# Performance work log

Measured on AMD Instinct MI355X. Metric: run time of the kernel, lower is better.

The kernel has to match this reference:

```python
import jax, jax.numpy as jnp
import numpy as np

B, S, H, DH, W, G, M = 2, 4096, 12, 64, 256, 64, 256
D = H * DH  # 768
VOCAB = 50282
NEG = -1e9


def setup_inputs() -> dict:
    key = jax.random.key(0)
    ks = jax.random.split(key, 16)
    f = lambda k, shp, s=0.02: jax.random.normal(k, shp, jnp.float32) * s
    return {
        'input_ids': jax.random.randint(ks[0], (B, S), 0, VOCAB, jnp.int32),
        'attn_mask': jnp.ones((B, S), jnp.float32),
        'html_idx': jnp.sort(jax.random.randint(ks[1], (B, M), 0, S, jnp.int32), axis=-1),
        'embed': f(ks[2], (VOCAB, D), 1.0),
        'Wq': f(ks[3], (D, D)), 'bq': jnp.zeros((D,), jnp.float32),
        'Wk': f(ks[4], (D, D)), 'bk': jnp.zeros((D,), jnp.float32),
        'Wv': f(ks[5], (D, D)), 'bv': jnp.zeros((D,), jnp.float32),
        'Wo': f(ks[6], (D, D)), 'bo': jnp.zeros((D,), jnp.float32),
        'gamma': jnp.ones((D,), jnp.float32), 'beta': jnp.zeros((D,), jnp.float32),
        'Wp': f(ks[7], (D, D)), 'bp': jnp.zeros((D,), jnp.float32),
        'Wa': f(ks[8], (D, 3)), 'ba': jnp.zeros((3,), jnp.float32),
        'Ws': f(ks[9], (D, 2)), 'bs': jnp.zeros((2,), jnp.float32),
    }


def _band_shift(t, n_chunks):
    # t: [..., n_chunks+2, W, ...chunked along axis -3/-2]; gather 3 neighbor chunks
    return jnp.concatenate([t[..., i:i + n_chunks, :, :] for i in range(3)], axis=-2)


def longformer_hpt(input_ids, attn_mask, html_idx, embed, Wq, bq, Wk, bk, Wv, bv,
                   Wo, bo, gamma, beta, Wp, bp, Wa, ba, Ws, bs):
    x = embed[input_ids]  # [B,S,D]
    heads = lambda t: t.reshape(B, S, H, DH).transpose(0, 2, 1, 3)  # [B,H,S,DH]
    q, k, v = heads(x @ Wq + bq), heads(x @ Wk + bk), heads(x @ Wv + bv)
    scale = 1.0 / np.sqrt(DH).astype(np.float32)
    C = S // W  # chunks

    # --- sliding-window (banded) attention, one-sided window W ---
    kp = jnp.pad(k, ((0, 0), (0, 0), (W, W), (0, 0))).reshape(B, H, C + 2, W, DH)
    vp = jnp.pad(v, ((0, 0), (0, 0), (W, W), (0, 0))).reshape(B, H, C + 2, W, DH)
    k3 = _band_shift(kp, C)  # [B,H,C,3W,DH]
    v3 = _band_shift(vp, C)
    qc = q.reshape(B, H, C, W, DH)
    sb = jnp.einsum('bhcqd,bhckd->bhcqk', qc, k3) * scale  # [B,H,C,W,3W]

    ii = jnp.arange(W)[:, None]
    jj = jnp.arange(3 * W)[None, :]
    band_ok = jnp.abs(jj - W - ii) <= W  # [W,3W]
    keypos = jnp.arange(C)[:, None] * W - W + jnp.arange(3 * W)[None, :]  # [C,3W]
    kvalid = (keypos >= 0) & (keypos < S) & (keypos >= G)  # global keys handled separately
    mp = jnp.pad(attn_mask, ((0, 0), (W, W))).reshape(B, C + 2, W)
    m3 = jnp.concatenate([mp[:, i:i + C] for i in range(3)], axis=2)  # [B,C,3W]
    mask = band_ok[None, :, :] & kvalid[:, None, :] & (m3[:, :, None, :] > 0)[..., :, :].reshape(B, C, 1, 3 * W).astype(bool) if False else (band_ok[None, None, :, :] & kvalid[None, :, None, :] & (m3[:, :, None, :] > 0))  # [B,C,W,3W]
    sb = jnp.where(mask[:, None], sb, NEG).reshape(B, H, S, 3 * W)

    # --- all tokens also attend to the G global tokens ---
    kg, vg = k[:, :, :G], v[:, :, :G]
    sg = jnp.einsum('bhsd,bhgd->bhsg', q, kg) * scale
    sg = jnp.where(attn_mask[:, None, None, :G] > 0, sg, NEG)

    p = jax.nn.softmax(jnp.concatenate([sg, sb], -1), -1)  # [B,H,S,G+3W]
    pg, pb = p[..., :G], p[..., G:].reshape(B, H, C, W, 3 * W)
    out = (jnp.einsum('bhcqk,bhckd->bhcqd', pb, v3).reshape(B, H, S, DH)
           + jnp.einsum('bhsg,bhgd->bhsd', pg, vg))

    # --- global queries attend to everything ---
    sgl = jnp.einsum('bhgd,bhsd->bhgs', q[:, :, :G], k) * scale
    sgl = jnp.where(attn_mask[:, None, None, :] > 0, sgl, NEG)
    outg = jnp.einsum('bhgs,bhsd->bhgd', jax.nn.softmax(sgl, -1), v)
    out = jnp.concatenate([outg, out[:, :, G:]], axis=2)

    ctx = out.transpose(0, 2, 1, 3).reshape(B, S, D)
    h = x + ctx @ Wo + bo
    mu = h.mean(-1, keepdims=True)
    var = ((h - mu) ** 2).mean(-1, keepdims=True)
    hn = (h - mu) / jnp.sqrt(var + 1e-5) * gamma + beta  # last_hidden [B,S,D]

    # probes (ans_probe: Linear(768,3)+Sigmoid, span_probe: Linear(768,2)+Sigmoid)
    ans = jax.nn.sigmoid(hn @ Wa + ba)
    span = jax.nn.sigmoid(hn @ Ws + bs)

    # ReIndexer gather of HTML-element hidden states + ConditionCalculator
    hr = jnp.take_along_axis(hn, html_idx[:, :, None].astype(jnp.int32), axis=1)  # [B,M,D]
    t = jax.nn.relu(hr @ Wp + bp)
    cond = jax.nn.sigmoid(jnp.einsum('bqh,bch->bcq', hr, t))  # [B,M,M]
    return hn, ans, span, cond


def reference(input_ids, attn_mask, html_idx, embed, Wq, bq, Wk, bk, Wv, bv,
              Wo, bo, gamma, beta, Wp, bp, Wa, ba, Ws, bs):
    return longformer_hpt(input_ids, attn_mask, html_idx, embed, Wq, bq, Wk, bk,
                          Wv, bv, Wo, bo, gamma, beta, Wp, bp, Wa, ba, Ws, bs)
```

## Files before the change

### kernel.cpp

```cpp
#include <hip/hip_runtime.h>

typedef unsigned short u16;
typedef unsigned int   u32;
typedef __attribute__((ext_vector_type(8))) short s8v;
typedef __attribute__((ext_vector_type(8))) unsigned short us8;
typedef __attribute__((ext_vector_type(4))) float f4v;

constexpr int BC  = 2;
constexpr int SL  = 4096;
constexpr int NH  = 12;
constexpr int HD  = 64;
constexpr int DM  = 768;
constexpr int WIN = 256;
constexpr int GLB = 64;
constexpr int QN  = 2304;
constexpr int KCH = 32;
constexpr float FOLD = 0.125f * 1.44269504088896f;
constexpr float NEGS = -1.0e9f;

__device__ __forceinline__ float b2f(u16 b){ return __uint_as_float(((u32)b) << 16); }
__device__ __forceinline__ u16 f2b(float f){
  u32 u = __float_as_uint(f);
  return (u16)((u + 0x7fffu + ((u >> 16) & 1u)) >> 16);
}
__device__ __forceinline__ float wredsum(float v){
  #pragma unroll
  for (int o = 32; o > 0; o >>= 1) v += __shfl_xor(v, o, 64);
  return v;
}
__device__ __forceinline__ float sigf(float x){ return 1.f / (1.f + __expf(-x)); }

__global__ void pack_embed(const float* __restrict__ Wq, const float* __restrict__ Wk,
                           const float* __restrict__ Wv, const float* __restrict__ Wo,
                           const float* __restrict__ Wp,
                           const float* __restrict__ bq, const float* __restrict__ bk,
                           const float* __restrict__ bv,
                           u16* __restrict__ wt_qkv, u16* __restrict__ wt_o,
                           u16* __restrict__ wt_p, float* __restrict__ b_qkv,
                           const int* __restrict__ ids, const float* __restrict__ emb,
                           u16* __restrict__ xb)
{
  __shared__ float tile[64][65];
  const int bid = blockIdx.x;
  const int t = threadIdx.x;
  if (bid < 720){
    const int mi = bid / 144, rest = bid % 144;
    const int kt = rest / 12, ntc = rest % 12;
    const float* src = (mi==0)?Wq:(mi==1)?Wk:(mi==2)?Wv:(mi==3)?Wo:Wp;
    u16* dst = (mi<3) ? (wt_qkv + (size_t)mi*768*768) : ((mi==3) ? wt_o : wt_p);
    const int k0 = kt*64, n0 = ntc*64;
    #pragma unroll
    for (int i=0;i<4;i++){
      const int r = (t>>4) + i*16;
      float4 v = ((const float4*)(src + (long)(k0+r)*768 + n0))[t&15];
      tile[r][(t&15)*4+0] = v.x; tile[r][(t&15)*4+1] = v.y;
      tile[r][(t&15)*4+2] = v.z; tile[r][(t&15)*4+3] = v.w;
    }
    __syncthreads();
    const int n = t & 63, kc = (t>>6)*16;
    u32* d32 = (u32*)(dst + (long)(n0+n)*768 + k0 + kc);
    #pragma unroll
    for (int i=0;i<8;i++){
      d32[i] = (u32)f2b(tile[kc+2*i][n]) | ((u32)f2b(tile[kc+2*i+1][n]) << 16);
    }
    if (bid < 9){
      const int i = bid*256 + t;
      if (i < 2304) b_qkv[i] = (i < 768) ? bq[i] : (i < 1536) ? bk[i-768] : bv[i-1536];
    }
  } else {
    int e4 = (bid-720)*256 + t;
    int row = e4 / 192, d4 = e4 - row*192;
    int id = ids[row];
    float4 v = ((const float4*)(emb + (long)id*768))[d4];
    u32 p0 = (u32)f2b(v.x) | ((u32)f2b(v.y) << 16);
    u32 p1 = (u32)f2b(v.z) | ((u32)f2b(v.w) << 16);
    ((u32*)(xb + (long)row*768))[d4*2]   = p0;
    ((u32*)(xb + (long)row*768))[d4*2+1] = p1;
  }
}

__global__ void gather_hr(const int* __restrict__ hidx, const float* __restrict__ hn,
                          u16* __restrict__ hrb){
  int e = blockIdx.x*256 + threadIdx.x;
  if (e >= 512*768) return;
  int r = e / 768, d = e - r*768;
  int b = r >> 8;
  int idx = hidx[r];
  hrb[e] = f2b(hn[((long)(b*SL + idx))*768 + d]);
}

template<int MODE, bool SWZ>
__global__ __launch_bounds__(256, 2)
void gemm_bt(const u16* __restrict__ A, const u16* __restrict__ Bt,
             const float* __restrict__ bias, const u16* __restrict__ resB,
             float* __restrict__ outF, u16* __restrict__ outB,
             int M, int N, int K, long sA, long sB, long sO)
{
  const int bz = blockIdx.z;
  A  += (long)bz * sA;
  Bt += (long)bz * sB;
  int vid = blockIdx.x + gridDim.x*blockIdx.y;
  if constexpr (SWZ){
    const int chunk = (gridDim.x*gridDim.y) >> 3;
    vid = (vid & 7)*chunk + (vid >> 3);
  }
  const int n0 = (vid % gridDim.x) * 128;
  const int m0 = (vid / gridDim.x) * 128;
  __shared__ u16 lsA[128*64];
  __shared__ u16 lsB[128*64];
  const int t = threadIdx.x;
  const int w = t >> 6, lane = t & 63;
  const int wr = w >> 1, wc = w & 1;
  const int fr = lane & 15, fq = lane >> 4;

  f4v acc[4][4];
  #pragma unroll
  for (int i=0;i<4;i++)
    #pragma unroll
    for (int j=0;j<4;j++) acc[i][j] = (f4v)0.f;

  for (int k0 = 0; k0 < K; k0 += 64){
    #pragma unroll
    for (int i=0;i<4;i++){
      int e = (w*4+i)*512 + lane*8;
      int row = e >> 6, col = e & 63;
      __builtin_amdgcn_global_load_lds(
        (const __attribute__((address_space(1))) void*)(A + (long)(m0+row)*K + (k0+col)),
        (__attribute__((address_space(3))) void*)(&lsA[(w*4+i)*512]), 16, 0, 0);
      __builtin_amdgcn_global_load_lds(
        (const __attribute__((address_space(1))) void*)(Bt + (long)(n0+row)*K + (k0+col)),
        (__attribute__((address_space(3))) void*)(&lsB[(w*4+i)*512]), 16, 0, 0);
    }
    __syncthreads();
    #pragma unroll
    for (int kk = 0; kk < 2; kk++){
      s8v af[4], bfv[4];
      #pragma unroll
      for (int mi=0;mi<4;mi++)
        af[mi] = *(const s8v*)&lsA[(wr*64 + mi*16 + fr)*64 + kk*32 + fq*8];
      #pragma unroll
      for (int ni=0;ni<4;ni++)
        bfv[ni] = *(const s8v*)&lsB[(wc*64 + ni*16 + fr)*64 + kk*32 + fq*8];
      #pragma unroll
      for (int mi=0;mi<4;mi++)
        #pragma unroll
        for (int ni=0;ni<4;ni++)
          acc[mi][ni] = __builtin_amdgcn_mfma_f32_16x16x32_bf16(af[mi], bfv[ni], acc[mi][ni], 0, 0, 0);
    }
    __syncthreads();
  }
  #pragma unroll
  for (int mi=0;mi<4;mi++){
    #pragma unroll
    for (int ni=0;ni<4;ni++){
      #pragma unroll
      for (int r=0;r<4;r++){
        int row = m0 + wr*64 + mi*16 + fq*4 + r;
        int col = n0 + wc*64 + ni*16 + fr;
        float v = acc[mi][ni][r];
        if constexpr (MODE == 0){
          v += bias[col];
          outB[(long)row*N + col] = f2b(v);
        } else if constexpr (MODE == 1){
          v += bias[col] + b2f(resB[(long)row*N + col]);
          outF[(long)row*N + col] = v;
        } else if constexpr (MODE == 2){
          v = fmaxf(v + bias[col], 0.f);
          outB[(long)row*N + col] = f2b(v);
        } else {
          (outF + bz*sO)[(long)row*N + col] = sigf(v);
        }
      }
    }
  }
}

__global__ __launch_bounds__(512, 2)
void attn_band_mfma(const u16* __restrict__ qkv, const float* __restrict__ mask, u16* __restrict__ ctx)
{
  const int bx = blockIdx.x;
  const int q0 = (((bx & 7) << 2) | (bx >> 3)) * 128;
  const int h = blockIdx.y, b = blockIdx.z;
  const int t = threadIdx.x;
  const int w = t >> 6, lane = t & 63;
  const int fq = lane >> 4, fr = lane & 15;
  const int qw = ((w >> 2) << 6) | ((w & 3) << 4);

  __shared__ u16 lsK[2][64*64];
  __shared__ u16 lsVT[2][64*72];
  __shared__ u16 lsP[8][16*72];
  __shared__ float lsM[2][64];

  const long bq = (long)b*SL*QN;
  const u16* qrow = qkv + (bq + (long)(q0 + qw + fr)*QN) + h*HD;
  s8v aq[2];
  aq[0] = *(const s8v*)(qrow + fq*8);
  aq[1] = *(const s8v*)(qrow + 32 + fq*8);

  const u16* kq = qkv + bq + DM + h*HD;
  const u16* vq = qkv + bq + 2*DM + h*HD;
  const float* mrow = mask + b*SL;

  const int kb0 = (q0 < 320) ? 64 : (q0 - 256);
  const int khi = (q0 + 384 < SL) ? (q0 + 384) : SL;
  const int NTT = 1 + ((khi - kb0) >> 6);

  f4v out[4];
  #pragma unroll
  for (int n=0;n<4;n++) out[n] = (f4v)0.f;
  float m[4]  = {-3.0e38f,-3.0e38f,-3.0e38f,-3.0e38f};
  float l[4]  = {0.f,0.f,0.f,0.f};

  us8 vv;
  auto stage_issue = [&](int i, int buf){
    const int k0 = (i == 0) ? 0 : kb0 + (i-1)*64;
    if (t < 64) lsM[buf][t] = mrow[k0 + t];
    const int r = w*8 + (lane>>3);
    const int d = ((lane&7) ^ (lane>>3))*8;
    __builtin_amdgcn_global_load_lds(
      (const __attribute__((address_space(1))) void*)(kq + (long)(k0+r)*QN + d),
      (__attribute__((address_space(3))) void*)(&lsK[buf][w*512]), 16, 0, 0);
    vv = *(const us8*)(vq + (long)(k0+lane)*QN + w*8);
  };

  stage_issue(0, 0);
  int cur = 0;
  for (int i = 0; i < NTT; i++){
    const int k0 = (i == 0) ? 0 : kb0 + (i-1)*64;
    const int d0 = w*8;
    #pragma unroll
    for (int jj=0;jj<8;jj++) lsVT[cur][(d0+jj)*72 + lane] = (u16)vv[jj];
    __syncthreads();
    if (i+1 < NTT) stage_issue(i+1, cur^1);

    f4v s[4];
    #pragma unroll
    for (int n=0;n<4;n++) s[n] = (f4v)0.f;
    __builtin_amdgcn_s_setprio(1);
    #pragma unroll
    for (int kk=0;kk<2;kk++){
      #pragma unroll
      for (int n=0;n<4;n++){
        s8v bf = *(const s8v*)&lsK[cur][(16*n+fr)*64 + (((kk*4+fq) ^ (fr&7))<<3)];
        s[n] = __builtin_amdgcn_mfma_f32_16x16x32_bf16(aq[kk], bf, s[n], 0,0,0);
      }
    }
    __builtin_amdgcn_s_setprio(0);
    const bool isg = (i == 0);
    #pragma unroll
    for (int n=0;n<4;n++){
      const int kcol = 16*n + fr;
      const float mk = lsM[cur][kcol];
      #pragma unroll
      for (int r=0;r<4;r++){
        const int dd = k0 + kcol - (q0 + qw + fq*4 + r);
        const bool valid = (mk > 0.f) && (isg || (dd >= -WIN && dd <= WIN));
        s[n][r] = valid ? s[n][r]*FOLD : NEGS;
      }
    }
    float rm[4];
    #pragma unroll
    for (int r=0;r<4;r++){
      float v = fmaxf(fmaxf(s[0][r], s[1][r]), fmaxf(s[2][r], s[3][r]));
      v = fmaxf(v, __shfl_xor(v, 1, 64));
      v = fmaxf(v, __shfl_xor(v, 2, 64));
      v = fmaxf(v, __shfl_xor(v, 4, 64));
      v = fmaxf(v, __shfl_xor(v, 8, 64));
      rm[r] = v;
    }
    bool need = false;
    #pragma unroll
    for (int r=0;r<4;r++) need |= (rm[r] > m[r] + 8.f);
    if (__any(need)){
      #pragma unroll
      for (int r=0;r<4;r++){
        const float mn = fmaxf(m[r], rm[r]);
        const float sf = exp2f(m[r] - mn);
        m[r] = mn;
        l[r] *= sf;
        #pragma unroll
        for (int n=0;n<4;n++) out[n][r] *= sf;
      }
    }
    u16* lsPw = lsP[w];
    float rs[4] = {0.f,0.f,0.f,0.f};
    #pragma unroll
    for (int n=0;n<4;n++){
      #pragma unroll
      for (int r=0;r<4;r++){
        float p = exp2f(s[n][r] - m[r]);
        rs[r] += p;
        lsPw[(fq*4+r)*72 + 16*n + fr] = f2b(p);
      }
    }
    #pragma unroll
    for (int r=0;r<4;r++){
      float rv = rs[r];
      rv += __shfl_xor(rv, 1, 64);
      rv += __shfl_xor(rv, 2, 64);
      rv += __shfl_xor(rv, 4, 64);
      rv += __shfl_xor(rv, 8, 64);
      l[r] += rv;
    }
    s8v ap[2];
    ap[0] = *(const s8v*)&lsPw[fr*72 + fq*8];
    ap[1] = *(const s8v*)&lsPw[fr*72 + 32 + fq*8];
    __builtin_amdgcn_s_setprio(1);
    #pragma unroll
    for (int kk=0;kk<2;kk++){
      #pragma unroll
      for (int n=0;n<4;n++){
        s8v bv = *(const s8v*)&lsVT[cur][(16*n+fr)*72 + kk*32 + fq*8];
        out[n] = __builtin_amdgcn_mfma_f32_16x16x32_bf16(ap[kk], bv, out[n], 0,0,0);
      }
    }
    __builtin_amdgcn_s_setprio(0);
    cur ^= 1;
  }
  #pragma unroll
  for (int r=0;r<4;r++) l[r] = 1.f/l[r];
  u16* cb = ctx + (((long)(b*SL) + q0 + qw + fq*4))*DM + h*HD + fr;
  #pragma unroll
  for (int n=0;n<4;n++)
    #pragma unroll
    for (int r=0;r<4;r++)
      cb[(long)r*DM + 16*n] = f2b(out[n][r]*l[r]);
}

__global__ __launch_bounds__(256, 3)
void attn_global_part(const u16* __restrict__ qkv, const float* __restrict__ mask,
                      float* __restrict__ pout, float* __restrict__ pml)
{
  const int ck = blockIdx.x;
  const int h = blockIdx.y, b = blockIdx.z;
  const int bh = b*NH + h;
  const int t = threadIdx.x;
  const int w = t >> 6, lane = t & 63;
  const int fq = lane >> 4, fr = lane & 15;

  __shared__ u16 lsK[2][64*64];
  __shared__ u16 lsVT[2][64*72];
  __shared__ u16 lsP[4][16*72];
  __shared__ float lsM[2][64];

  const long bq = (long)b*SL*QN;
  const u16* qrow = qkv + (bq + (long)(w*16 + fr)*QN) + h*HD;
  s8v aq[2];
  aq[0] = *(const s8v*)(qrow + fq*8);
  aq[1] = *(const s8v*)(qrow + 32 + fq*8);

  const u16* kq = qkv + bq + DM + h*HD;
  const u16* vq = qkv + bq + 2*DM + h*HD;
  const float* mrow = mask + b*SL;

  f4v out[4];
  #pragma unroll
  for (int n=0;n<4;n++) out[n] = (f4v)0.f;
  float m[4]  = {-3.0e38f,-3.0e38f,-3.0e38f,-3.0e38f};
  float l[4]  = {0.f,0.f,0.f,0.f};

  us8 vv0, vv1;
  auto stage_issue = [&](int i, int buf){
    const int k0 = ck*128 + i*64;
    if (t < 64) lsM[buf][t] = mrow[k0 + t];
    #pragma unroll
    for (int j=0;j<2;j++){
      const int r = (w*2+j)*8 + (lane>>3);
      const int d = ((lane&7) ^ (lane>>3))*8;
      __builtin_amdgcn_global_load_lds(
        (const __attribute__((address_space(1))) void*)(kq + (long)(k0+r)*QN + d),
        (__attribute__((address_space(3))) void*)(&lsK[buf][(w*2+j)*512]), 16, 0, 0);
    }
    vv0 = *(const us8*)(vq + (long)(k0+lane)*QN + w*8);
    vv1 = *(const us8*)(vq + (long)(k0+lane)*QN + w*8 + 32);
  };

  stage_issue(0, 0);
  int cur = 0;
  for (int i = 0; i < 2; i++){
    const int d0 = w*8;
    #pragma unroll
    for (int jj=0;jj<8;jj++) lsVT[cur][(d0+jj)*72 + lane] = (u16)vv0[jj];
    #pragma unroll
    for (int jj=0;jj<8;jj++) lsVT[cur][(d0+32+jj)*72 + lane] = (u16)vv1[jj];
    __syncthreads();
    if (i+1 < 2) stage_issue(i+1, cur^1);

    f4v s[4];
    #pragma unroll
    for (int n=0;n<4;n++) s[n] = (f4v)0.f;
    __builtin_amdgcn_s_setprio(1);
    #pragma unroll
    for (int kk=0;kk<2;kk++){
      #pragma unroll
      for (int n=0;n<4;n++){
        s8v bf = *(const s8v*)&lsK[cur][(16*n+fr)*64 + (((kk*4+fq) ^ (fr&7))<<3)];
        s[n] = __builtin_amdgcn_mfma_f32_16x16x32_bf16(aq[kk], bf, s[n], 0,0,0);
      }
    }
    __builtin_amdgcn_s_setprio(0);
    #pragma unroll
    for (int n=0;n<4;n++){
      const float mk = lsM[cur][16*n + fr];
      #pragma unroll
      for (int r=0;r<4;r++)
        s[n][r] = (mk > 0.f) ? s[n][r]*FOLD : NEGS;
    }
    float sf[4];
    #pragma unroll
    for (int r=0;r<4;r++){
      float rm = fmaxf(fmaxf(s[0][r], s[1][r]), fmaxf(s[2][r], s[3][r]));
      rm = fmaxf(rm, __shfl_xor(rm, 1, 64));
      rm = fmaxf(rm, __shfl_xor(rm, 2, 64));
      rm = fmaxf(rm, __shfl_xor(rm, 4, 64));
      rm = fmaxf(rm, __shfl_xor(rm, 8, 64));
      const float mn = fmaxf(m[r], rm);
      sf[r] = exp2f(m[r] - mn);
      m[r] = mn;
    }
    u16* lsPw = lsP[w];
    float rs[4] = {0.f,0.f,0.f,0.f};
    #pragma unroll
    for (int n=0;n<4;n++){
      #pragma unroll
      for (int r=0;r<4;r++){
        float p = exp2f(s[n][r] - m[r]);
        rs[r] += p;
        lsPw[(fq*4+r)*72 + 16*n + fr] = f2b(p);
        out[n][r] *= sf[r];
      }
    }
    #pragma unroll
    for (int r=0;r<4;r++){
      float rv = rs[r];
      rv += __shfl_xor(rv, 1, 64);
      rv += __shfl_xor(rv, 2, 64);
      rv += __shfl_xor(rv, 4, 64);
      rv += __shfl_xor(rv, 8, 64);
      l[r] = l[r]*sf[r] + rv;
    }
    s8v ap[2];
    ap[0] = *(const s8v*)&lsPw[fr*72 + fq*8];
    ap[1] = *(const s8v*)&lsPw[fr*72 + 32 + fq*8];
    __builtin_amdgcn_s_setprio(1);
    #pragma unroll
    for (int kk=0;kk<2;kk++){
      #pragma unroll
      for (int n=0;n<4;n++){
        s8v bv = *(const s8v*)&lsVT[cur][(16*n+fr)*72 + kk*32 + fq*8];
        out[n] = __builtin_amdgcn_mfma_f32_16x16x32_bf16(ap[kk], bv, out[n], 0,0,0);
      }
    }
    __builtin_amdgcn_s_setprio(0);
    cur ^= 1;
  }
  float* pob = pout + ((long)(ck*BC*NH + bh))*64*64;
  #pragma unroll
  for (int n=0;n<4;n++)
    #pragma unroll
    for (int r=0;r<4;r++)
      pob[(w*16 + fq*4 + r)*64 + 16*n + fr] = out[n][r];
  if (fr == 0){
    float* pmb = pml + ((long)(ck*BC*NH + bh))*128;
    #pragma unroll
    for (int r=0;r<4;r++){
      pmb[(w*16 + fq*4 + r)*2 + 0] = m[r];
      pmb[(w*16 + fq*4 + r)*2 + 1] = l[r];
    }
  }
}

__global__ __launch_bounds__(256, 2)
void attn_global_combine(const float* __restrict__ pout, const float* __restrict__ pml,
                         u16* __restrict__ ctx)
{
  const int bh = blockIdx.x;
  const int b = bh / NH, h = bh % NH;
  const int t = threadIdx.x;
  __shared__ float wgt[KCH][64];
  __shared__ float rl[64];
  if (t < 64){
    float mc[KCH], lc[KCH];
    #pragma unroll
    for (int c = 0; c < KCH; c++){
      const float* pmb = pml + ((long)(c*BC*NH + bh))*128 + t*2;
      mc[c] = pmb[0]; lc[c] = pmb[1];
    }
    float M = mc[0];
    #pragma unroll
    for (int c = 1; c < KCH; c++) M = fmaxf(M, mc[c]);
    float L = 0.f;
    #pragma unroll
    for (int c = 0; c < KCH; c++){
      const float wv = exp2f(mc[c] - M);
      wgt[c][t] = wv;
      L += lc[c]*wv;
    }
    rl[t] = 1.f/L;
  }
  __syncthreads();
  const int row = t >> 2, dseg = t & 3;
  float acc[16];
  #pragma unroll
  for (int i=0;i<16;i++) acc[i] = 0.f;
  for (int c = 0; c < KCH; c++){
    const float wv = wgt[c][row];
    const float4* pb = (const float4*)(pout + ((long)(c*BC*NH + bh)*64 + row)*64 + dseg*16);
    #pragma unroll
    for (int i = 0; i < 4; i++){
      float4 v = pb[i];
      acc[i*4+0] += v.x*wv; acc[i*4+1] += v.y*wv;
      acc[i*4+2] += v.z*wv; acc[i*4+3] += v.w*wv;
    }
  }
  u16* cr = ctx + ((long)(b*SL + row))*DM + h*HD + dseg*16;
  const float r = rl[row];
  #pragma unroll
  for (int i = 0; i < 16; i += 2){
    u32 pk = (u32)f2b(acc[i]*r) | ((u32)f2b(acc[i+1]*r) << 16);
    *(u32*)(cr + i) = pk;
  }
}

__global__ __launch_bounds__(256, 2)
void ln_heads(const float* __restrict__ hbuf, const float* __restrict__ gamma, const float* __restrict__ beta,
              const float* __restrict__ Wa, const float* __restrict__ ba,
              const float* __restrict__ Wsp, const float* __restrict__ bsp,
              float* __restrict__ hn, float* __restrict__ ans, float* __restrict__ span)
{
  const int r = blockIdx.x;
  const int t = threadIdx.x, lane = t & 63, w = t >> 6;
  __shared__ float red[8];
  __shared__ float dred[4][5];
  const float* hrow = hbuf + (long)r*DM;
  float v0 = hrow[t], v1 = hrow[t+256], v2 = hrow[t+512];
  float sum = wredsum(v0 + v1 + v2);
  float sq  = wredsum(v0*v0 + v1*v1 + v2*v2);
  if (lane == 0){ red[w] = sum; red[4+w] = sq; }
  __syncthreads();
  const float mu  = (red[0]+red[1]+red[2]+red[3]) * (1.f/768.f);
  const float msq = (red[4]+red[5]+red[6]+red[7]) * (1.f/768.f);
  const float rstd = rsqrtf(msq - mu*mu + 1e-5f);
  float pa0=0,pa1=0,pa2=0,ps0=0,ps1=0;
  const long base = (long)r*DM;
  #pragma unroll
  for (int jj = 0; jj < 3; jj++){
    const int i = t + jj*256;
    const float hv = (jj==0) ? v0 : (jj==1) ? v1 : v2;
    const float y = (hv - mu)*rstd*gamma[i] + beta[i];
    hn[base + i] = y;
    pa0 += y*Wa[i*3+0]; pa1 += y*Wa[i*3+1]; pa2 += y*Wa[i*3+2];
    ps0 += y*Wsp[i*2+0]; ps1 += y*Wsp[i*2+1];
  }
  pa0 = wredsum(pa0); pa1 = wredsum(pa1); pa2 = wredsum(pa2);
  ps0 = wredsum(ps0); ps1 = wredsum(ps1);
  if (lane == 0){ dred[w][0]=pa0; dred[w][1]=pa1; dred[w][2]=pa2; dred[w][3]=ps0; dred[w][4]=ps1; }
  __syncthreads();
  if (t == 0){
    float A0 = dred[0][0]+dred[1][0]+dred[2][0]+dred[3][0];
    float A1 = dred[0][1]+dred[1][1]+dred[2][1]+dred[3][1];
    float A2 = dred[0][2]+dred[1][2]+dred[2][2]+dred[3][2];
    float S0 = dred[0][3]+dred[1][3]+dred[2][3]+dred[3][3];
    float S1 = dred[0][4]+dred[1][4]+dred[2][4]+dred[3][4];
    ans[(long)r*3+0]  = sigf(A0 + ba[0]);
    ans[(long)r*3+1]  = sigf(A1 + ba[1]);
    ans[(long)r*3+2]  = sigf(A2 + ba[2]);
    span[(long)r*2+0] = sigf(S0 + bsp[0]);
    span[(long)r*2+1] = sigf(S1 + bsp[1]);
  }
}

extern "C" void kernel_launch(void* const* d_in, const int* in_sizes, int n_in,
                              void* d_out, int out_size, void* d_ws, size_t ws_size,
                              hipStream_t stream)
{
  const int*   input_ids = (const int*)  d_in[0];
  const float* attn_mask = (const float*)d_in[1];
  const int*   html_idx  = (const int*)  d_in[2];
  const float* embed     = (const float*)d_in[3];
  const float* Wq = (const float*)d_in[4];  const float* bq = (const float*)d_in[5];
  const float* Wk = (const float*)d_in[6];  const float* bk = (const float*)d_in[7];
  const float* Wv = (const float*)d_in[8];  const float* bv = (const float*)d_in[9];
  const float* Wo = (const float*)d_in[10]; const float* bo = (const float*)d_in[11];
  const float* gamma = (const float*)d_in[12]; const float* beta = (const float*)d_in[13];
  const float* Wp = (const float*)d_in[14]; const float* bp = (const float*)d_in[15];
  const float* Wa = (const float*)d_in[16]; const float* ba = (const float*)d_in[17];
  const float* Wsp = (const float*)d_in[18]; const float* bsp = (const float*)d_in[19];

  char* ws = (char*)d_ws;
  size_t off = 0;
  auto take = [&](size_t bytes)->char*{
    char* p = ws + off; off += (bytes + 255) & ~(size_t)255; return p;
  };
  u16*   x_b    = (u16*)  take((size_t)8192*768*2);
  u16*   wt_qkv = (u16*)  take((size_t)2304*768*2);
  u16*   wt_o   = (u16*)  take((size_t)768*768*2);
  u16*   wt_p   = (u16*)  take((size_t)768*768*2);
  float* b_qkv  = (float*)take(2304*4);
  u16*   qkv_b  = (u16*)  take((size_t)8192*2304*2);
  u16*   ctx_b  = (u16*)  take((size_t)8192*768*2);
  float* h_f    = (float*)take((size_t)8192*768*4);
  u16*   hr_b   = (u16*)  take((size_t)512*768*2);
  u16*   t_b    = (u16*)  take((size_t)512*768*2);
  float* pout   = (float*)take((size_t)KCH*BC*NH*64*64*4);
  float* pml    = (float*)take((size_t)KCH*BC*NH*128*4);

  float* out_hn   = (float*)d_out;
  float* out_ans  = out_hn  + (size_t)8192*768;
  float* out_span = out_ans + (size_t)8192*3;
  float* out_cond = out_span + (size_t)8192*2;

  pack_embed<<<6864, 256, 0, stream>>>(Wq, Wk, Wv, Wo, Wp, bq, bk, bv,
                                       wt_qkv, wt_o, wt_p, b_qkv,
                                       input_ids, embed, x_b);

  gemm_bt<0,true><<<dim3(18,64,1), 256, 0, stream>>>(x_b, wt_qkv, b_qkv, nullptr,
                                                nullptr, qkv_b, 8192, 2304, 768, 0,0,0);
  attn_band_mfma<<<dim3(32,12,2), 512, 0, stream>>>(qkv_b, attn_mask, ctx_b);
  attn_global_part<<<dim3(KCH,12,2), 256, 0, stream>>>(qkv_b, attn_mask, pout, pml);
  attn_global_combine<<<BC*NH, 256, 0, stream>>>(pout, pml, ctx_b);
  gemm_bt<1,true><<<dim3(6,64,1), 256, 0, stream>>>(ctx_b, wt_o, bo, x_b,
                                               h_f, nullptr, 8192, 768, 768, 0,0,0);
  ln_heads<<<8192, 256, 0, stream>>>(h_f, gamma, beta, Wa, ba, Wsp, bsp,
                                     out_hn, out_ans, out_span);
  gather_hr<<<1536, 256, 0, stream>>>(html_idx, out_hn, hr_b);
  gemm_bt<2,false><<<dim3(6,4,1), 256, 0, stream>>>(hr_b, wt_p, bp, nullptr,
                                              nullptr, t_b, 512, 768, 768, 0,0,0);
  gemm_bt<3,false><<<dim3(2,2,2), 256, 0, stream>>>(t_b, hr_b, nullptr, nullptr,
                                              out_cond, nullptr, 256, 256, 768,
                                              (long)256*768, (long)256*768, (long)256*256);
}
```

Measured before the change: 235.1 us.

## Fuse band and global attention into one launch; store pre-LN residual as bf16

```diff
diff --git a/kernel.cpp b/kernel.cpp
--- a/kernel.cpp
+++ b/kernel.cpp
@@ -163,7 +163,7 @@
           outB[(long)row*N + col] = f2b(v);
         } else if constexpr (MODE == 1){
           v += bias[col] + b2f(resB[(long)row*N + col]);
-          outF[(long)row*N + col] = v;
+          outB[(long)row*N + col] = f2b(v);
         } else if constexpr (MODE == 2){
           v = fmaxf(v + bias[col], 0.f);
           outB[(long)row*N + col] = f2b(v);
@@ -175,35 +175,26 @@
   }
 }
 
-__global__ __launch_bounds__(512, 2)
-void attn_band_mfma(const u16* __restrict__ qkv, const float* __restrict__ mask, u16* __restrict__ ctx)
+__global__ __launch_bounds__(256, 3)
+void attn_fused(const u16* __restrict__ qkv, const float* __restrict__ mask,
+                u16* __restrict__ ctx, float* __restrict__ pout, float* __restrict__ pml)
 {
   const int bx = blockIdx.x;
-  const int q0 = (((bx & 7) << 2) | (bx >> 3)) * 128;
+  const int vid = (bx & 7)*12 + (bx >> 3);
   const int h = blockIdx.y, b = blockIdx.z;
   const int t = threadIdx.x;
   const int w = t >> 6, lane = t & 63;
   const int fq = lane >> 4, fr = lane & 15;
-  const int qw = ((w >> 2) << 6) | ((w & 3) << 4);
 
   __shared__ u16 lsK[2][64*64];
   __shared__ u16 lsVT[2][64*72];
-  __shared__ u16 lsP[8][16*72];
+  __shared__ u16 lsP[4][16*72];
   __shared__ float lsM[2][64];
 
   const long bq = (long)b*SL*QN;
-  const u16* qrow = qkv + (bq + (long)(q0 + qw + fr)*QN) + h*HD;
-  s8v aq[2];
-  aq[0] = *(const s8v*)(qrow + fq*8);
-  aq[1] = *(const s8v*)(qrow + 32 + fq*8);
-
   const u16* kq = qkv + bq + DM + h*HD;
   const u16* vq = qkv + bq + 2*DM + h*HD;
   const float* mrow = mask + b*SL;
-
-  const int kb0 = (q0 < 320) ? 64 : (q0 - 256);
-  const int khi = (q0 + 384 < SL) ? (q0 + 384) : SL;
-  const int NTT = 1 + ((khi - kb0) >> 6);
 
   f4v out[4];
   #pragma unroll
@@ -211,261 +202,256 @@
   float m[4]  = {-3.0e38f,-3.0e38f,-3.0e38f,-3.0e38f};
   float l[4]  = {0.f,0.f,0.f,0.f};
 
-  us8 vv;
-  auto stage_issue = [&](int i, int buf){
-    const int k0 = (i == 0) ? 0 : kb0 + (i-1)*64;
-    if (t < 64) lsM[buf][t] = mrow[k0 + t];
-    const int r = w*8 + (lane>>3);
-    const int d = ((lane&7) ^ (lane>>3))*8;
-    __builtin_amdgcn_global_load_lds(
-      (const __attribute__((address_space(1))) void*)(kq + (long)(k0+r)*QN + d),
-      (__attribute__((address_space(3))) void*)(&lsK[buf][w*512]), 16, 0, 0);
-    vv = *(const us8*)(vq + (long)(k0+lane)*QN + w*8);
-  };
-
-  stage_issue(0, 0);
-  int cur = 0;
-  for (int i = 0; i < NTT; i++){
-    const int k0 = (i == 0) ? 0 : kb0 + (i-1)*64;
-    const int d0 = w*8;
-    #pragma unroll
-    for (int jj=0;jj<8;jj++) lsVT[cur][(d0+jj)*72 + lane] = (u16)vv[jj];
-    __syncthreads();
-    if (i+1 < NTT) stage_issue(i+1, cur^1);
-
-    f4v s[4];
-    #pragma unroll
-    for (int n=0;n<4;n++) s[n] = (f4v)0.f;
-    __builtin_amdgcn_s_setprio(1);
-    #pragma unroll
-    for (int kk=0;kk<2;kk++){
+  us8 vv0, vv1;
+
+  if (vid < 64){
+    const int q0 = vid * 64;
+    const u16* qrow = qkv + (bq + (long)(q0 + w*16 + fr)*QN) + h*HD;
+    s8v aq[2];
+    aq[0] = *(const s8v*)(qrow + fq*8);
+    aq[1] = *(const s8v*)(qrow + 32 + fq*8);
+
+    const int ti_lo = (q0 < 320) ? ((320 - q0) >> 6) : 0;
+    const int ti_hi_raw = (4352 - q0) >> 6;
+    const int ti_hi = ti_hi_raw < 9 ? ti_hi_raw : 9;
+    const int NTT = 1 + (ti_hi - ti_lo);
+    const int kb0 = q0 - 256 + ti_lo*64;
+
+    auto stage_issue = [&](int i, int buf){
+      const int k0 = (i == 0) ? 0 : kb0 + (i-1)*64;
+      if (t < 64) lsM[buf][t] = mrow[k0 + t];
+      #pragma unroll
+      for (int j=0;j<2;j++){
+        const int r = (w*2+j)*8 + (lane>>3);
+        const int d = ((lane&7) ^ (lane>>3))*8;
+        __builtin_amdgcn_global_load_lds(
+          (const __attribute__((address_space(1))) void*)(kq + (long)(k0+r)*QN + d),
+          (__attribute__((address_space(3))) void*)(&lsK[buf][(w*2+j)*512]), 16, 0, 0);
+      }
+      vv0 = *(const us8*)(vq + (long)(k0+lane)*QN + w*8);
+      vv1 = *(const us8*)(vq + (long)(k0+lane)*QN + w*8 + 32);
+    };
+
+    stage_issue(0, 0);
+    int cur = 0;
+    for (int i = 0; i < NTT; i++){
+      const int k0 = (i == 0) ? 0 : kb0 + (i-1)*64;
+      const int d0 = w*8;
+      #pragma unroll
+      for (int jj=0;jj<8;jj++) lsVT[cur][(d0+jj)*72 + lane] = (u16)vv0[jj];
+      #pragma unroll
+      for (int jj=0;jj<8;jj++) lsVT[cur][(d0+32+jj)*72 + lane] = (u16)vv1[jj];
+      __syncthreads();
+      if (i+1 < NTT) stage_issue(i+1, cur^1);
+
+      f4v s[4];
+      #pragma unroll
+      for (int n=0;n<4;n++) s[n] = (f4v)0.f;
+      __builtin_amdgcn_s_setprio(1);
+      #pragma unroll
+      for (int kk=0;kk<2;kk++){
+        #pragma unroll
+        for (int n=0;n<4;n++){
+          s8v bf = *(const s8v*)&lsK[cur][(16*n+fr)*64 + (((kk*4+fq) ^ (fr&7))<<3)];
+          s[n] = __builtin_amdgcn_mfma_f32_16x16x32_bf16(aq[kk], bf, s[n], 0,0,0);
+        }
+      }
+      __builtin_amdgcn_s_setprio(0);
+      const bool isg = (i == 0);
       #pragma unroll
       for (int n=0;n<4;n++){
-        s8v bf = *(const s8v*)&lsK[cur][(16*n+fr)*64 + (((kk*4+fq) ^ (fr&7))<<3)];
-        s[n] = __builtin_amdgcn_mfma_f32_16x16x32_bf16(aq[kk], bf, s[n], 0,0,0);
-      }
-    }
-    __builtin_amdgcn_s_setprio(0);
-    const bool isg = (i == 0);
-    #pragma unroll
-    for (int n=0;n<4;n++){
-      const int kcol = 16*n + fr;
-      const float mk = lsM[cur][kcol];
+        const int kcol = 16*n + fr;
+        const float mk = lsM[cur][kcol];
+        #pragma unroll
+        for (int r=0;r<4;r++){
+          const int dd = k0 + kcol - (q0 + w*16 + fq*4 + r);
+          const bool valid = (mk > 0.f) && (isg || (dd >= -WIN && dd <= WIN));
+          s[n][r] = valid ? s[n][r]*FOLD : NEGS;
+        }
+      }
+      float rm[4];
       #pragma unroll
       for (int r=0;r<4;r++){
-        const int dd = k0 + kcol - (q0 + qw + fq*4 + r);
-        const bool valid = (mk > 0.f) && (isg || (dd >= -WIN && dd <= WIN));
-        s[n][r] = valid ? s[n][r]*FOLD : NEGS;
-      }
-    }
-    float rm[4];
-    #pragma unroll
-    for (int r=0;r<4;r++){
-      float v = fmaxf(fmaxf(s[0][r], s[1][r]), fmaxf(s[2][r], s[3][r]));
-      v = fmaxf(v, __shfl_xor(v, 1, 64));
-      v = fmaxf(v, __shfl_xor(v, 2, 64));
-      v = fmaxf(v, __shfl_xor(v, 4, 64));
-      v = fmaxf(v, __shfl_xor(v, 8, 64));
-      rm[r] = v;
-    }
-    bool need = false;
-    #pragma unroll
-    for (int r=0;r<4;r++) need |= (rm[r] > m[r] + 8.f);
-    if (__any(need)){
+        float v = fmaxf(fmaxf(s[0][r], s[1][r]), fmaxf(s[2][r], s[3][r]));
+        v = fmaxf(v, __shfl_xor(v, 1, 64));
+        v = fmaxf(v, __shfl_xor(v, 2, 64));
+        v = fmaxf(v, __shfl_xor(v, 4, 64));
+        v = fmaxf(v, __shfl_xor(v, 8, 64));
+        rm[r] = v;
+      }
+      bool need = false;
+      #pragma unroll
+      for (int r=0;r<4;r++) need |= (rm[r] > m[r] + 8.f);
+      if (__any(need)){
+        #pragma unroll
+        for (int r=0;r<4;r++){
+          const float mn = fmaxf(m[r], rm[r]);
+          const float sf = exp2f(m[r] - mn);
+          m[r] = mn;
+          l[r] *= sf;
+          #pragma unroll
+          for (int n=0;n<4;n++) out[n][r] *= sf;
+        }
+      }
+      u16* lsPw = lsP[w];
+      float rs[4] = {0.f,0.f,0.f,0.f};
+      #pragma unroll
+      for (int n=0;n<4;n++){
+        #pragma unroll
+        for (int r=0;r<4;r++){
+          float p = exp2f(s[n][r] - m[r]);
+          rs[r] += p;
+          lsPw[(fq*4+r)*72 + 16*n + fr] = f2b(p);
+        }
+      }
       #pragma unroll
       for (int r=0;r<4;r++){
-        const float mn = fmaxf(m[r], rm[r]);
-        const float sf = exp2f(m[r] - mn);
+        float rv = rs[r];
+        rv += __shfl_xor(rv, 1, 64);
+        rv += __shfl_xor(rv, 2, 64);
+        rv += __shfl_xor(rv, 4, 64);
+        rv += __shfl_xor(rv, 8, 64);
+        l[r] += rv;
+      }
+      s8v ap[2];
+      ap[0] = *(const s8v*)&lsPw[fr*72 + fq*8];
+      ap[1] = *(const s8v*)&lsPw[fr*72 + 32 + fq*8];
+      __builtin_amdgcn_s_setprio(1);
+      #pragma unroll
+      for (int kk=0;kk<2;kk++){
+        #pragma unroll
+        for (int n=0;n<4;n++){
+          s8v bv = *(const s8v*)&lsVT[cur][(16*n+fr)*72 + kk*32 + fq*8];
+          out[n] = __builtin_amdgcn_mfma_f32_16x16x32_bf16(ap[kk], bv, out[n], 0,0,0);
+        }
+      }
+      __builtin_amdgcn_s_setprio(0);
+      cur ^= 1;
+    }
+    #pragma unroll
+    for (int r=0;r<4;r++) l[r] = 1.f/l[r];
+    u16* cb = ctx + (((long)(b*SL) + q0 + w*16 + fq*4))*DM + h*HD + fr;
+    #pragma unroll
+    for (int n=0;n<4;n++)
+      #pragma unroll
+      for (int r=0;r<4;r++)
+        cb[(long)r*DM + 16*n] = f2b(out[n][r]*l[r]);
+
+  } else {
+    const int ck = vid - 64;
+    const int bh = b*NH + h;
+    const u16* qrow = qkv + (bq + (long)(w*16 + fr)*QN) + h*HD;
+    s8v aq[2];
+    aq[0] = *(const s8v*)(qrow + fq*8);
+    aq[1] = *(const s8v*)(qrow + 32 + fq*8);
+
+    auto stage_issue = [&](int i, int buf){
+      const int k0 = ck*128 + i*64;
+      if (t < 64) lsM[buf][t] = mrow[k0 + t];
+      #pragma unroll
+      for (int j=0;j<2;j++){
+        const int r = (w*2+j)*8 + (lane>>3);
+        const int d = ((lane&7) ^ (lane>>3))*8;
+        __builtin_amdgcn_global_load_lds(
+          (const __attribute__((address_space(1))) void*)(kq + (long)(k0+r)*QN + d),
+          (__attribute__((address_space(3))) void*)(&lsK[buf][(w*2+j)*512]), 16, 0, 0);
+      }
+      vv0 = *(const us8*)(vq + (long)(k0+lane)*QN + w*8);
+      vv1 = *(const us8*)(vq + (long)(k0+lane)*QN + w*8 + 32);
+    };
+
+    stage_issue(0, 0);
+    int cur = 0;
+    for (int i = 0; i < 2; i++){
+      const int d0 = w*8;
+      #pragma unroll
+      for (int jj=0;jj<8;jj++) lsVT[cur][(d0+jj)*72 + lane] = (u16)vv0[jj];
+      #pragma unroll
+      for (int jj=0;jj<8;jj++) lsVT[cur][(d0+32+jj)*72 + lane] = (u16)vv1[jj];
+      __syncthreads();
+      if (i+1 < 2) stage_issue(i+1, cur^1);
+
+      f4v s[4];
+      #pragma unroll
+      for (int n=0;n<4;n++) s[n] = (f4v)0.f;
+      __builtin_amdgcn_s_setprio(1);
+      #pragma unroll
+      for (int kk=0;kk<2;kk++){
+        #pragma unroll
+        for (int n=0;n<4;n++){
+          s8v bf = *(const s8v*)&lsK[cur][(16*n+fr)*64 + (((kk*4+fq) ^ (fr&7))<<3)];
+          s[n] = __builtin_amdgcn_mfma_f32_16x16x32_bf16(aq[kk], bf, s[n], 0,0,0);
+        }
+      }
+      __builtin_amdgcn_s_setprio(0);
+      #pragma unroll
+      for (int n=0;n<4;n++){
+        const float mk = lsM[cur][16*n + fr];
+        #pragma unroll
+        for (int r=0;r<4;r++)
+          s[n][r] = (mk > 0.f) ? s[n][r]*FOLD : NEGS;
+      }
+      float sf[4];
+      #pragma unroll
+      for (int r=0;r<4;r++){
+        float rm = fmaxf(fmaxf(s[0][r], s[1][r]), fmaxf(s[2][r], s[3][r]));
+        rm = fmaxf(rm, __shfl_xor(rm, 1, 64));
+        rm = fmaxf(rm, __shfl_xor(rm, 2, 64));
+        rm = fmaxf(rm, __shfl_xor(rm, 4, 64));
+        rm = fmaxf(rm, __shfl_xor(rm, 8, 64));
+        const float mn = fmaxf(m[r], rm);
+        sf[r] = exp2f(m[r] - mn);
         m[r] = mn;
-        l[r] *= sf;
-        #pragma unroll
-        for (int n=0;n<4;n++) out[n][r] *= sf;
-      }
-    }
-    u16* lsPw = lsP[w];
-    float rs[4] = {0.f,0.f,0.f,0.f};
-    #pragma unroll
-    for (int n=0;n<4;n++){
+      }
+      u16* lsPw = lsP[w];
+      float rs[4] = {0.f,0.f,0.f,0.f};
+      #pragma unroll
+      for (int n=0;n<4;n++){
+        #pragma unroll
+        for (int r=0;r<4;r++){
+          float p = exp2f(s[n][r] - m[r]);
+          rs[r] += p;
+          lsPw[(fq*4+r)*72 + 16*n + fr] = f2b(p);
+          out[n][r] *= sf[r];
+        }
+      }
       #pragma unroll
       for (int r=0;r<4;r++){
-        float p = exp2f(s[n][r] - m[r]);
-        rs[r] += p;
-        lsPw[(fq*4+r)*72 + 16*n + fr] = f2b(p);
-      }
-    }
-    #pragma unroll
-    for (int r=0;r<4;r++){
-      float rv = rs[r];
-      rv += __shfl_xor(rv, 1, 64);
-      rv += __shfl_xor(rv, 2, 64);
-      rv += __shfl_xor(rv, 4, 64);
-      rv += __shfl_xor(rv, 8, 64);
-      l[r] += rv;
-    }
-    s8v ap[2];
-    ap[0] = *(const s8v*)&lsPw[fr*72 + fq*8];
-    ap[1] = *(const s8v*)&lsPw[fr*72 + 32 + fq*8];
-    __builtin_amdgcn_s_setprio(1);
-    #pragma unroll
-    for (int kk=0;kk<2;kk++){
-      #pragma unroll
-      for (int n=0;n<4;n++){
-        s8v bv = *(const s8v*)&lsVT[cur][(16*n+fr)*72 + kk*32 + fq*8];
-        out[n] = __builtin_amdgcn_mfma_f32_16x16x32_bf16(ap[kk], bv, out[n], 0,0,0);
-      }
-    }
-    __builtin_amdgcn_s_setprio(0);
-    cur ^= 1;
-  }
-  #pragma unroll
-  for (int r=0;r<4;r++) l[r] = 1.f/l[r];
-  u16* cb = ctx + (((long)(b*SL) + q0 + qw + fq*4))*DM + h*HD + fr;
-  #pragma unroll
-  for (int n=0;n<4;n++)
-    #pragma unroll
-    for (int r=0;r<4;r++)
-      cb[(long)r*DM + 16*n] = f2b(out[n][r]*l[r]);
-}
-
-__global__ __launch_bounds__(256, 3)
-void attn_global_part(const u16* __restrict__ qkv, const float* __restrict__ mask,
-                      float* __restrict__ pout, float* __restrict__ pml)
-{
-  const int ck = blockIdx.x;
-  const int h = blockIdx.y, b = blockIdx.z;
-  const int bh = b*NH + h;
-  const int t = threadIdx.x;
-  const int w = t >> 6, lane = t & 63;
-  const int fq = lane >> 4, fr = lane & 15;
-
-  __shared__ u16 lsK[2][64*64];
-  __shared__ u16 lsVT[2][64*72];
-  __shared__ u16 lsP[4][16*72];
-  __shared__ float lsM[2][64];
-
-  const long bq = (long)b*SL*QN;
-  const u16* qrow = qkv + (bq + (long)(w*16 + fr)*QN) + h*HD;
-  s8v aq[2];
-  aq[0] = *(const s8v*)(qrow + fq*8);
-  aq[1] = *(const s8v*)(qrow + 32 + fq*8);
-
-  const u16* kq = qkv + bq + DM + h*HD;
-  const u16* vq = qkv + bq + 2*DM + h*HD;
-  const float* mrow = mask + b*SL;
-
-  f4v out[4];
-  #pragma unroll
-  for (int n=0;n<4;n++) out[n] = (f4v)0.f;
-  float m[4]  = {-3.0e38f,-3.0e38f,-3.0e38f,-3.0e38f};
-  float l[4]  = {0.f,0.f,0.f,0.f};
-
-  us8 vv0, vv1;
-  auto stage_issue = [&](int i, int buf){
-    const int k0 = ck*128 + i*64;
-    if (t < 64) lsM[buf][t] = mrow[k0 + t];
-    #pragma unroll
-    for (int j=0;j<2;j++){
-      const int r = (w*2+j)*8 + (lane>>3);
-      const int d = ((lane&7) ^ (lane>>3))*8;
-      __builtin_amdgcn_global_load_lds(
-        (const __attribute__((address_space(1))) void*)(kq + (long)(k0+r)*QN + d),
-        (__attribute__((address_space(3))) void*)(&lsK[buf][(w*2+j)*512]), 16, 0, 0);
-    }
-    vv0 = *(const us8*)(vq + (long)(k0+lane)*QN + w*8);
-    vv1 = *(const us8*)(vq + (long)(k0+lane)*QN + w*8 + 32);
-  };
-
-  stage_issue(0, 0);
-  int cur = 0;
-  for (int i = 0; i < 2; i++){
-    const int d0 = w*8;
-    #pragma unroll
-    for (int jj=0;jj<8;jj++) lsVT[cur][(d0+jj)*72 + lane] = (u16)vv0[jj];
-    #pragma unroll
-    for (int jj=0;jj<8;jj++) lsVT[cur][(d0+32+jj)*72 + lane] = (u16)vv1[jj];
-    __syncthreads();
-    if (i+1 < 2) stage_issue(i+1, cur^1);
-
-    f4v s[4];
-    #pragma unroll
-    for (int n=0;n<4;n++) s[n] = (f4v)0.f;
-    __builtin_amdgcn_s_setprio(1);
-    #pragma unroll
-    for (int kk=0;kk<2;kk++){
-      #pragma unroll
-      for (int n=0;n<4;n++){
-        s8v bf = *(const s8v*)&lsK[cur][(16*n+fr)*64 + (((kk*4+fq) ^ (fr&7))<<3)];
-        s[n] = __builtin_amdgcn_mfma_f32_16x16x32_bf16(aq[kk], bf, s[n], 0,0,0);
-      }
-    }
-    __builtin_amdgcn_s_setprio(0);
-    #pragma unroll
-    for (int n=0;n<4;n++){
-      const float mk = lsM[cur][16*n + fr];
+        float rv = rs[r];
+        rv += __shfl_xor(rv, 1, 64);
+        rv += __shfl_xor(rv, 2, 64);
+        rv += __shfl_xor(rv, 4, 64);
+        rv += __shfl_xor(rv, 8, 64);
+        l[r] = l[r]*sf[r] + rv;
+      }
+      s8v ap[2];
+      ap[0] = *(const s8v*)&lsPw[fr*72 + fq*8];
+      ap[1] = *(const s8v*)&lsPw[fr*72 + 32 + fq*8];
+      __builtin_amdgcn_s_setprio(1);
+      #pragma unroll
+      for (int kk=0;kk<2;kk++){
+        #pragma unroll
+        for (int n=0;n<4;n++){
+          s8v bv = *(const s8v*)&lsVT[cur][(16*n+fr)*72 + kk*32 + fq*8];
+          out[n] = __builtin_amdgcn_mfma_f32_16x16x32_bf16(ap[kk], bv, out[n], 0,0,0);
+        }
+      }
+      __builtin_amdgcn_s_setprio(0);
+      cur ^= 1;
+    }
+    float* pob = pout + ((long)(ck*BC*NH + bh))*64*64;
+    #pragma unroll
+    for (int n=0;n<4;n++)
       #pragma unroll
       for (int r=0;r<4;r++)
-        s[n][r] = (mk > 0.f) ? s[n][r]*FOLD : NEGS;
-    }
-    float sf[4];
-    #pragma unroll
-    for (int r=0;r<4;r++){
-      float rm = fmaxf(fmaxf(s[0][r], s[1][r]), fmaxf(s[2][r], s[3][r]));
-      rm = fmaxf(rm, __shfl_xor(rm, 1, 64));
-      rm = fmaxf(rm, __shfl_xor(rm, 2, 64));
-      rm = fmaxf(rm, __shfl_xor(rm, 4, 64));
-      rm = fmaxf(rm, __shfl_xor(rm, 8, 64));
-      const float mn = fmaxf(m[r], rm);
-      sf[r] = exp2f(m[r] - mn);
-      m[r] = mn;
-    }
-    u16* lsPw = lsP[w];
-    float rs[4] = {0.f,0.f,0.f,0.f};
-    #pragma unroll
-    for (int n=0;n<4;n++){
+        pob[(w*16 + fq*4 + r)*64 + 16*n + fr] = out[n][r];
+    if (fr == 0){
+      float* pmb = pml + ((long)(ck*BC*NH + bh))*128;
       #pragma unroll
       for (int r=0;r<4;r++){
-        float p = exp2f(s[n][r] - m[r]);
-        rs[r] += p;
-        lsPw[(fq*4+r)*72 + 16*n + fr] = f2b(p);
-        out[n][r] *= sf[r];
-      }
-    }
-    #pragma unroll
-    for (int r=0;r<4;r++){
-      float rv = rs[r];
-      rv += __shfl_xor(rv, 1, 64);
-      rv += __shfl_xor(rv, 2, 64);
-      rv += __shfl_xor(rv, 4, 64);
-      rv += __shfl_xor(rv, 8, 64);
-      l[r] = l[r]*sf[r] + rv;
-    }
-    s8v ap[2];
-    ap[0] = *(const s8v*)&lsPw[fr*72 + fq*8];
-    ap[1] = *(const s8v*)&lsPw[fr*72 + 32 + fq*8];
-    __builtin_amdgcn_s_setprio(1);
-    #pragma unroll
-    for (int kk=0;kk<2;kk++){
-      #pragma unroll
-      for (int n=0;n<4;n++){
-        s8v bv = *(const s8v*)&lsVT[cur][(16*n+fr)*72 + kk*32 + fq*8];
-        out[n] = __builtin_amdgcn_mfma_f32_16x16x32_bf16(ap[kk], bv, out[n], 0,0,0);
-      }
-    }
-    __builtin_amdgcn_s_setprio(0);
-    cur ^= 1;
-  }
-  float* pob = pout + ((long)(ck*BC*NH + bh))*64*64;
-  #pragma unroll
-  for (int n=0;n<4;n++)
-    #pragma unroll
-    for (int r=0;r<4;r++)
-      pob[(w*16 + fq*4 + r)*64 + 16*n + fr] = out[n][r];
-  if (fr == 0){
-    float* pmb = pml + ((long)(ck*BC*NH + bh))*128;
-    #pragma unroll
-    for (int r=0;r<4;r++){
-      pmb[(w*16 + fq*4 + r)*2 + 0] = m[r];
-      pmb[(w*16 + fq*4 + r)*2 + 1] = l[r];
+        pmb[(w*16 + fq*4 + r)*2 + 0] = m[r];
+        pmb[(w*16 + fq*4 + r)*2 + 1] = l[r];
+      }
     }
   }
 }
@@ -522,46 +508,45 @@
   }
 }
 
-__global__ __launch_bounds__(256, 2)
-void ln_heads(const float* __restrict__ hbuf, const float* __restrict__ gamma, const float* __restrict__ beta,
+__global__ __launch_bounds__(384, 2)
+void ln_heads(const u16* __restrict__ hb, const float* __restrict__ gamma, const float* __restrict__ beta,
               const float* __restrict__ Wa, const float* __restrict__ ba,
               const float* __restrict__ Wsp, const float* __restrict__ bsp,
               float* __restrict__ hn, float* __restrict__ ans, float* __restrict__ span)
 {
   const int r = blockIdx.x;
   const int t = threadIdx.x, lane = t & 63, w = t >> 6;
-  __shared__ float red[8];
-  __shared__ float dred[4][5];
-  const float* hrow = hbuf + (long)r*DM;
-  float v0 = hrow[t], v1 = hrow[t+256], v2 = hrow[t+512];
-  float sum = wredsum(v0 + v1 + v2);
-  float sq  = wredsum(v0*v0 + v1*v1 + v2*v2);
-  if (lane == 0){ red[w] = sum; red[4+w] = sq; }
+  __shared__ float red[12];
+  __shared__ float dred[6][5];
+  const u32 pk = ((const u32*)(hb + (long)r*DM))[t];
+  const float v0 = b2f((u16)(pk & 0xffff));
+  const float v1 = b2f((u16)(pk >> 16));
+  float sum = wredsum(v0 + v1);
+  float sq  = wredsum(v0*v0 + v1*v1);
+  if (lane == 0){ red[w] = sum; red[6+w] = sq; }
   __syncthreads();
-  const float mu  = (red[0]+red[1]+red[2]+red[3]) * (1.f/768.f);
-  const float msq = (red[4]+red[5]+red[6]+red[7]) * (1.f/768.f);
+  float mu = 0.f, msq = 0.f;
+  #pragma unroll
+  for (int i=0;i<6;i++){ mu += red[i]; msq += red[6+i]; }
+  mu *= (1.f/768.f); msq *= (1.f/768.f);
   const float rstd = rsqrtf(msq - mu*mu + 1e-5f);
-  float pa0=0,pa1=0,pa2=0,ps0=0,ps1=0;
-  const long base = (long)r*DM;
-  #pragma unroll
-  for (int jj = 0; jj < 3; jj++){
-    const int i = t + jj*256;
-    const float hv = (jj==0) ? v0 : (jj==1) ? v1 : v2;
-    const float y = (hv - mu)*rstd*gamma[i] + beta[i];
-    hn[base + i] = y;
-    pa0 += y*Wa[i*3+0]; pa1 += y*Wa[i*3+1]; pa2 += y*Wa[i*3+2];
-    ps0 += y*Wsp[i*2+0]; ps1 += y*Wsp[i*2+1];
-  }
+  const int i0 = 2*t, i1 = 2*t+1;
+  const float y0 = (v0 - mu)*rstd*gamma[i0] + beta[i0];
+  const float y1 = (v1 - mu)*rstd*gamma[i1] + beta[i1];
+  ((float2*)(hn + (long)r*DM))[t] = make_float2(y0, y1);
+  float pa0 = y0*Wa[i0*3+0] + y1*Wa[i1*3+0];
+  float pa1 = y0*Wa[i0*3+1] + y1*Wa[i1*3+1];
+  float pa2 = y0*Wa[i0*3+2] + y1*Wa[i1*3+2];
+  float ps0 = y0*Wsp[i0*2+0] + y1*Wsp[i1*2+0];
+  float ps1 = y0*Wsp[i0*2+1] + y1*Wsp[i1*2+1];
   pa0 = wredsum(pa0); pa1 = wredsum(pa1); pa2 = wredsum(pa2);
   ps0 = wredsum(ps0); ps1 = wredsum(ps1);
   if (lane == 0){ dred[w][0]=pa0; dred[w][1]=pa1; dred[w][2]=pa2; dred[w][3]=ps0; dred[w][4]=ps1; }
   __syncthreads();
   if (t == 0){
-    float A0 = dred[0][0]+dred[1][0]+dred[2][0]+dred[3][0];
-    float A1 = dred[0][1]+dred[1][1]+dred[2][1]+dred[3][1];
-    float A2 = dred[0][2]+dred[1][2]+dred[2][2]+dred[3][2];
-    float S0 = dred[0][3]+dred[1][3]+dred[2][3]+dred[3][3];
-    float S1 = dred[0][4]+dred[1][4]+dred[2][4]+dred[3][4];
+    float A0=0,A1=0,A2=0,S0=0,S1=0;
+    #pragma unroll
+    for (int i=0;i<6;i++){ A0+=dred[i][0]; A1+=dred[i][1]; A2+=dred[i][2]; S0+=dred[i][3]; S1+=dred[i][4]; }
     ans[(long)r*3+0]  = sigf(A0 + ba[0]);
     ans[(long)r*3+1]  = sigf(A1 + ba[1]);
     ans[(long)r*3+2]  = sigf(A2 + ba[2]);
@@ -599,7 +584,7 @@
   float* b_qkv  = (float*)take(2304*4);
   u16*   qkv_b  = (u16*)  take((size_t)8192*2304*2);
   u16*   ctx_b  = (u16*)  take((size_t)8192*768*2);
-  float* h_f    = (float*)take((size_t)8192*768*4);
+  u16*   h_b    = (u16*)  take((size_t)8192*768*2);
   u16*   hr_b   = (u16*)  take((size_t)512*768*2);
   u16*   t_b    = (u16*)  take((size_t)512*768*2);
   float* pout   = (float*)take((size_t)KCH*BC*NH*64*64*4);
@@ -616,12 +601,11 @@
 
   gemm_bt<0,true><<<dim3(18,64,1), 256, 0, stream>>>(x_b, wt_qkv, b_qkv, nullptr,
                                                 nullptr, qkv_b, 8192, 2304, 768, 0,0,0);
-  attn_band_mfma<<<dim3(32,12,2), 512, 0, stream>>>(qkv_b, attn_mask, ctx_b);
-  attn_global_part<<<dim3(KCH,12,2), 256, 0, stream>>>(qkv_b, attn_mask, pout, pml);
+  attn_fused<<<dim3(96,12,2), 256, 0, stream>>>(qkv_b, attn_mask, ctx_b, pout, pml);
   attn_global_combine<<<BC*NH, 256, 0, stream>>>(pout, pml, ctx_b);
   gemm_bt<1,true><<<dim3(6,64,1), 256, 0, stream>>>(ctx_b, wt_o, bo, x_b,
-                                               h_f, nullptr, 8192, 768, 768, 0,0,0);
-  ln_heads<<<8192, 256, 0, stream>>>(h_f, gamma, beta, Wa, ba, Wsp, bsp,
+                                               nullptr, h_b, 8192, 768, 768, 0,0,0);
+  ln_heads<<<8192, 384, 0, stream>>>(h_b, gamma, beta, Wa, ba, Wsp, bsp,
                                      out_hn, out_ans, out_span);
   gather_hr<<<1536, 256, 0, stream>>>(html_idx, out_hn, hr_b);
   gemm_bt<2,false><<<dim3(6,4,1), 256, 0, stream>>>(hr_b, wt_p, bp, nullptr,
```

Measured after the change: 260.8 us. 10.9% more time.
